# Kernel optimization log

Hardware: AMD Instinct MI355X
Metric: run time of the kernel (lower is better)

## Reference

```python
import jax, jax.numpy as jnp
import numpy as np

L, B, D = 8192, 4096, 1024


def setup_inputs() -> dict:
    key = jax.random.key(0)
    k1, k2, k3, k4 = jax.random.split(key, 4)
    return {
        "q_hat": jax.random.normal(k1, (L, D), dtype=jnp.float32),
        "q_real": jax.random.normal(k2, (L, D), dtype=jnp.float32),
        "encoded_gt": jax.random.normal(k3, (B, D), dtype=jnp.float32),
        "encoded_pred": jax.random.normal(k4, (B, D), dtype=jnp.float32),
    }


def reference(q_hat, q_real, encoded_gt, encoded_pred):
    # local_loss: -(1/L) * sum_i dot(q_hat[i], q_real[i])
    # (replaces the Python loop of L tiny torch.dot launches with one fused reduce)
    local = -jnp.mean(jnp.sum(q_hat * q_real, axis=-1))

    # global_loss: sum_{i,j} max(0, <pred_i, gt_j> - <pred_i, gt_i> + 1)
    # (replaces the O(B^2) double loop of torch.dot calls with one GEMM)
    scores = jnp.einsum("id,jd->ij", encoded_pred, encoded_gt)  # [B, B]
    pos = jnp.diagonal(scores)                                   # [B]
    margin = jnp.float32(1.0)
    glob = jnp.sum(jnp.maximum(0.0, scores - pos[:, None] + margin))

    return local + glob
```

## Files before the change

### kernel.cpp

```cpp
#include <hip/hip_runtime.h>
#include <hip/hip_bf16.h>

#define LROWS 8192
#define BROWS 4096
#define DDIM  1024

typedef __attribute__((ext_vector_type(4)))  int   i32x4;
typedef __attribute__((ext_vector_type(8)))  int   i32x8;
typedef __attribute__((ext_vector_type(16))) float f32x16;

typedef const unsigned int __attribute__((address_space(1))) gu32;
typedef unsigned int       __attribute__((address_space(3))) su32;

__device__ inline unsigned int pack_fp8x4(float4 v) {
    unsigned int w = 0;
    w = __builtin_amdgcn_cvt_pk_fp8_f32(v.x, v.y, w, false);
    w = __builtin_amdgcn_cvt_pk_fp8_f32(v.z, v.w, w, true);
    return w;
}

__global__ __launch_bounds__(256) void prep_kernel(
    const float4* __restrict__ pred,
    const float4* __restrict__ gt,
    unsigned int* __restrict__ opred,
    unsigned int* __restrict__ ogt,
    const float4* __restrict__ qh,
    const float4* __restrict__ qr,
    float* __restrict__ pos,
    float* __restrict__ lpart,
    float* __restrict__ out) {
    __shared__ float sred[4], sred2[4];
    const int row = blockIdx.x;
    const int t = threadIdx.x;
    if (row == 0 && t == 0) out[0] = 0.0f;

    const int idx = row * 256 + t;
    float4 p = pred[idx];
    float4 g = gt[idx];
    opred[idx] = pack_fp8x4(p);
    ogt[idx]   = pack_fp8x4(g);
    float s = p.x * g.x + p.y * g.y + p.z * g.z + p.w * g.w;

    const int qi = row * 512 + t;
    float4 a0 = qh[qi], b0 = qr[qi];
    float4 a1 = qh[qi + 256], b1 = qr[qi + 256];
    float ls = a0.x * b0.x + a0.y * b0.y + a0.z * b0.z + a0.w * b0.w
             + a1.x * b1.x + a1.y * b1.y + a1.z * b1.z + a1.w * b1.w;

    #pragma unroll
    for (int o = 32; o > 0; o >>= 1) {
        s  += __shfl_down(s, o, 64);
        ls += __shfl_down(ls, o, 64);
    }
    if ((t & 63) == 0) { sred[t >> 6] = s; sred2[t >> 6] = ls; }
    __syncthreads();
    if (t == 0) {
        pos[row]   = sred[0] + sred[1] + sred[2] + sred[3];
        lpart[row] = sred2[0] + sred2[1] + sred2[2] + sred2[3];
    }
}

__global__ __launch_bounds__(256) void hinge_gemm(
    const unsigned char* __restrict__ A,
    const unsigned char* __restrict__ Bm,
    const float* __restrict__ pos,
    const float* __restrict__ lpart,
    float* __restrict__ out) {
    __shared__ unsigned char As[128 * 128];
    __shared__ unsigned char Bs[128 * 128];
    __shared__ float pos_s[128];
    __shared__ float sred[4];

    const int bm = blockIdx.y;
    const int bn = blockIdx.x;
    const int tid = threadIdx.x;
    const int lane = tid & 63;
    const int wave = tid >> 6;
    const int wm = wave >> 1;
    const int wn = wave & 1;

    if (tid < 128) pos_s[tid] = pos[bm * 128 + tid];

    const int grow = lane >> 3;
    const int usw  = (lane & 7) ^ grow;

    const unsigned char* Abase = A + (size_t)(bm * 128) * DDIM;
    const unsigned char* Bbase = Bm + (size_t)(bn * 128) * DDIM;

    f32x16 acc[2][2];
    #pragma unroll
    for (int i = 0; i < 2; i++)
        #pragma unroll
        for (int j = 0; j < 2; j++)
            #pragma unroll
            for (int r = 0; r < 16; r++) acc[i][j][r] = 0.0f;

    const int sc1 = 0x7f7f7f7f;
    const int mrow = lane & 31;
    const int kh = lane >> 5;

    for (int k0 = 0; k0 < DDIM; k0 += 128) {
        #pragma unroll
        for (int i = 0; i < 4; i++) {
            int c = wave * 4 + i;
            int row = c * 8 + grow;
            __builtin_amdgcn_global_load_lds(
                (gu32*)(Abase + (size_t)row * DDIM + k0 + usw * 16),
                (su32*)(As + c * 1024), 16, 0, 0);
            __builtin_amdgcn_global_load_lds(
                (gu32*)(Bbase + (size_t)row * DDIM + k0 + usw * 16),
                (su32*)(Bs + c * 1024), 16, 0, 0);
        }
        __syncthreads();

        #pragma unroll
        for (int h = 0; h < 2; h++) {
            const int u0 = h * 4 + kh * 2;
            i32x8 af[2], bg[2];
            #pragma unroll
            for (int mt = 0; mt < 2; mt++) {
                int r = wm * 64 + mt * 32 + mrow;
                i32x4 x0 = *(const i32x4*)&As[r * 128 + ((u0    ) ^ (r & 7)) * 16];
                i32x4 x1 = *(const i32x4*)&As[r * 128 + ((u0 + 1) ^ (r & 7)) * 16];
                af[mt] = __builtin_shufflevector(x0, x1, 0, 1, 2, 3, 4, 5, 6, 7);
            }
            #pragma unroll
            for (int nt = 0; nt < 2; nt++) {
                int r = wn * 64 + nt * 32 + mrow;
                i32x4 x0 = *(const i32x4*)&Bs[r * 128 + ((u0    ) ^ (r & 7)) * 16];
                i32x4 x1 = *(const i32x4*)&Bs[r * 128 + ((u0 + 1) ^ (r & 7)) * 16];
                bg[nt] = __builtin_shufflevector(x0, x1, 0, 1, 2, 3, 4, 5, 6, 7);
            }
            #pragma unroll
            for (int mt = 0; mt < 2; mt++)
                #pragma unroll
                for (int nt = 0; nt < 2; nt++)
                    acc[mt][nt] = __builtin_amdgcn_mfma_scale_f32_32x32x64_f8f6f4(
                        af[mt], bg[nt], acc[mt][nt],
                        0, 0,
                        0, sc1,
                        0, sc1);
        }
        __syncthreads();
    }

    float s = 0.0f;
    const int rq = 4 * (lane >> 5);
    #pragma unroll
    for (int mt = 0; mt < 2; mt++) {
        #pragma unroll
        for (int nt = 0; nt < 2; nt++) {
            #pragma unroll
            for (int i = 0; i < 16; i++) {
                int lr = wm * 64 + mt * 32 + (i & 3) + 8 * (i >> 2) + rq;
                float v = acc[mt][nt][i] - pos_s[lr] + 1.0f;
                s += fmaxf(v, 0.0f);
            }
        }
    }
    #pragma unroll
    for (int o = 32; o > 0; o >>= 1) s += __shfl_down(s, o, 64);
    if (lane == 0) sred[wave] = s;
    __syncthreads();
    if (tid == 0) {
        const int bid = (bm * 32 + bn) * 4;
        float lp = lpart[bid] + lpart[bid + 1] + lpart[bid + 2] + lpart[bid + 3];
        atomicAdd(out, sred[0] + sred[1] + sred[2] + sred[3]
                       - lp * (1.0f / (float)LROWS));
    }
}

extern "C" void kernel_launch(void* const* d_in, const int* in_sizes, int n_in,
                              void* d_out, int out_size, void* d_ws, size_t ws_size,
                              hipStream_t stream) {
    const float* q_hat  = (const float*)d_in[0];
    const float* q_real = (const float*)d_in[1];
    const float* gt     = (const float*)d_in[2];
    const float* pred   = (const float*)d_in[3];
    float* out = (float*)d_out;

    char* ws = (char*)d_ws;
    unsigned char* pred_8 = (unsigned char*)ws;
    unsigned char* gt_8   = (unsigned char*)(ws + (size_t)BROWS * DDIM);
    float* pos   = (float*)(ws + (size_t)2 * BROWS * DDIM);
    float* lpart = (float*)(ws + (size_t)2 * BROWS * DDIM + BROWS * 4);

    hipLaunchKernelGGL(prep_kernel, dim3(BROWS), dim3(256), 0, stream,
                       (const float4*)pred, (const float4*)gt,
                       (unsigned int*)pred_8, (unsigned int*)gt_8,
                       (const float4*)q_hat, (const float4*)q_real,
                       pos, lpart, out);

    hipLaunchKernelGGL(hinge_gemm, dim3(32, 32), dim3(256), 0, stream,
                       pred_8, gt_8, pos, lpart, out);
}
```

Before: 146.6 us.

## Double-buffer LDS tiles with 64-wide K steps and prefetch next tile

The GEMM main loop now uses two 8 KB LDS buffers per operand with a K step of 64. It issues global_load_lds for the next K slice before the MFMAs on the current slice, so there is one barrier per iteration instead of two. The LDS layout and XOR swizzle are reworked to pack two rows per 128-byte line. The aim is to hide global-to-LDS latency behind compute. In exchange there are twice as many loop iterations, each with less work, and the new swizzle carries some risk of bank conflicts or indexing errors.

```diff
diff --git a/kernel.cpp b/kernel.cpp
--- a/kernel.cpp
+++ b/kernel.cpp
@@ -66,8 +66,8 @@
     const float* __restrict__ pos,
     const float* __restrict__ lpart,
     float* __restrict__ out) {
-    __shared__ unsigned char As[128 * 128];
-    __shared__ unsigned char Bs[128 * 128];
+    __shared__ unsigned char As[2][8192];
+    __shared__ unsigned char Bs[2][8192];
     __shared__ float pos_s[128];
     __shared__ float sred[4];
 
@@ -81,8 +81,10 @@
 
     if (tid < 128) pos_s[tid] = pos[bm * 128 + tid];
 
-    const int grow = lane >> 3;
-    const int usw  = (lane & 7) ^ grow;
+    const int j8  = lane >> 3;
+    const int sl  = (lane & 7) ^ j8;
+    const int str = j8 * 2 + (sl >> 2);
+    const int suo = (sl & 3) * 16;
 
     const unsigned char* Abase = A + (size_t)(bm * 128) * DDIM;
     const unsigned char* Bbase = Bm + (size_t)(bn * 128) * DDIM;
@@ -97,51 +99,68 @@
 
     const int sc1 = 0x7f7f7f7f;
     const int mrow = lane & 31;
-    const int kh = lane >> 5;
-
-    for (int k0 = 0; k0 < DDIM; k0 += 128) {
-        #pragma unroll
-        for (int i = 0; i < 4; i++) {
-            int c = wave * 4 + i;
-            int row = c * 8 + grow;
-            __builtin_amdgcn_global_load_lds(
-                (gu32*)(Abase + (size_t)row * DDIM + k0 + usw * 16),
-                (su32*)(As + c * 1024), 16, 0, 0);
-            __builtin_amdgcn_global_load_lds(
-                (gu32*)(Bbase + (size_t)row * DDIM + k0 + usw * 16),
-                (su32*)(Bs + c * 1024), 16, 0, 0);
-        }
+    const int kh   = lane >> 5;
+
+    const int m_hi = mrow >> 1;
+    const int slot = ((kh * 2) | ((mrow & 1) << 2)) ^ (m_hi & 7);
+    const int aoff0 = (wm * 32 + m_hi) * 128 + slot * 16;
+    const int boff0 = (wn * 32 + m_hi) * 128 + slot * 16;
+
+    #pragma unroll
+    for (int c2 = 0; c2 < 2; c2++) {
+        int c = wave * 2 + c2;
+        int trow = c * 16 + str;
+        __builtin_amdgcn_global_load_lds(
+            (gu32*)(Abase + (size_t)trow * DDIM + suo),
+            (su32*)(As[0] + c * 1024), 16, 0, 0);
+        __builtin_amdgcn_global_load_lds(
+            (gu32*)(Bbase + (size_t)trow * DDIM + suo),
+            (su32*)(Bs[0] + c * 1024), 16, 0, 0);
+    }
+
+    #pragma unroll
+    for (int i = 0; i < 16; i++) {
         __syncthreads();
-
-        #pragma unroll
-        for (int h = 0; h < 2; h++) {
-            const int u0 = h * 4 + kh * 2;
-            i32x8 af[2], bg[2];
-            #pragma unroll
-            for (int mt = 0; mt < 2; mt++) {
-                int r = wm * 64 + mt * 32 + mrow;
-                i32x4 x0 = *(const i32x4*)&As[r * 128 + ((u0    ) ^ (r & 7)) * 16];
-                i32x4 x1 = *(const i32x4*)&As[r * 128 + ((u0 + 1) ^ (r & 7)) * 16];
-                af[mt] = __builtin_shufflevector(x0, x1, 0, 1, 2, 3, 4, 5, 6, 7);
+        const int cur = i & 1, nxt = cur ^ 1;
+        if (i < 15) {
+            const int k1 = (i + 1) * 64;
+            #pragma unroll
+            for (int c2 = 0; c2 < 2; c2++) {
+                int c = wave * 2 + c2;
+                int trow = c * 16 + str;
+                __builtin_amdgcn_global_load_lds(
+                    (gu32*)(Abase + (size_t)trow * DDIM + k1 + suo),
+                    (su32*)(As[nxt] + c * 1024), 16, 0, 0);
+                __builtin_amdgcn_global_load_lds(
+                    (gu32*)(Bbase + (size_t)trow * DDIM + k1 + suo),
+                    (su32*)(Bs[nxt] + c * 1024), 16, 0, 0);
             }
-            #pragma unroll
-            for (int nt = 0; nt < 2; nt++) {
-                int r = wn * 64 + nt * 32 + mrow;
-                i32x4 x0 = *(const i32x4*)&Bs[r * 128 + ((u0    ) ^ (r & 7)) * 16];
-                i32x4 x1 = *(const i32x4*)&Bs[r * 128 + ((u0 + 1) ^ (r & 7)) * 16];
-                bg[nt] = __builtin_shufflevector(x0, x1, 0, 1, 2, 3, 4, 5, 6, 7);
-            }
-            #pragma unroll
-            for (int mt = 0; mt < 2; mt++)
-                #pragma unroll
-                for (int nt = 0; nt < 2; nt++)
-                    acc[mt][nt] = __builtin_amdgcn_mfma_scale_f32_32x32x64_f8f6f4(
-                        af[mt], bg[nt], acc[mt][nt],
-                        0, 0,
-                        0, sc1,
-                        0, sc1);
-        }
-        __syncthreads();
+        }
+
+        i32x8 af[2], bg[2];
+        #pragma unroll
+        for (int mt = 0; mt < 2; mt++) {
+            int o = aoff0 + mt * 2048;
+            i32x4 x0 = *(const i32x4*)&As[cur][o];
+            i32x4 x1 = *(const i32x4*)&As[cur][o ^ 16];
+            af[mt] = __builtin_shufflevector(x0, x1, 0, 1, 2, 3, 4, 5, 6, 7);
+        }
+        #pragma unroll
+        for (int nt = 0; nt < 2; nt++) {
+            int o = boff0 + nt * 2048;
+            i32x4 x0 = *(const i32x4*)&Bs[cur][o];
+            i32x4 x1 = *(const i32x4*)&Bs[cur][o ^ 16];
+            bg[nt] = __builtin_shufflevector(x0, x1, 0, 1, 2, 3, 4, 5, 6, 7);
+        }
+        #pragma unroll
+        for (int mt = 0; mt < 2; mt++)
+            #pragma unroll
+            for (int nt = 0; nt < 2; nt++)
+                acc[mt][nt] = __builtin_amdgcn_mfma_scale_f32_32x32x64_f8f6f4(
+                    af[mt], bg[nt], acc[mt][nt],
+                    0, 0,
+                    0, sc1,
+                    0, sc1);
     }
 
     float s = 0.0f;
```

New measurement: 147.7 us. Within noise of the previous version (+0.8%).
